# Kernel tuning notes

Hardware: AMD Instinct MI355X
Metric: run time of the kernel (lower is better)

## Reference

```python
import jax, jax.numpy as jnp
import numpy as np

B, TQ, TK = 2, 2048, 2048
H, E, D = 16, 256, 4096       # num_heads, embed_dim, d_model
DH = D // H                   # head_dim == embed_dim (required by per-head RMSNorm(embed_dim))
LAMBDA_INIT = 0.8
LAYER_INDEX = 0
EPS = 1.1920929e-07           # torch RMSNorm default eps = finfo(float32).eps


def setup_inputs() -> dict:
    key = jax.random.key(0)
    ks = jax.random.split(key, 14)
    s = 0.02
    lam_init_val = LAMBDA_INIT - 0.6 * float(np.exp(-0.3 * LAYER_INDEX))
    return {
        "x": jax.random.normal(ks[0], (B, TQ, E), jnp.float32),
        "encoder_out": jax.random.normal(ks[1], (B, TK, E), jnp.float32),
        "Wq": jax.random.normal(ks[2], (H, E, DH), jnp.float32) * s,
        "bq": jnp.zeros((H, DH), jnp.float32),
        "Wk": jax.random.normal(ks[3], (H, E, DH), jnp.float32) * s,
        "bk": jnp.zeros((H, DH), jnp.float32),
        "Wv": jax.random.normal(ks[4], (H, E, DH), jnp.float32) * s,
        "bv": jnp.zeros((H, DH), jnp.float32),
        "lq1": jax.random.normal(ks[5], (H, DH), jnp.float32) * 0.1,
        "lk1": jax.random.normal(ks[6], (H, DH), jnp.float32) * 0.1,
        "lq2": jax.random.normal(ks[7], (H, DH), jnp.float32) * 0.1,
        "lk2": jax.random.normal(ks[8], (H, DH), jnp.float32) * 0.1,
        "lam_init": jnp.full((H,), lam_init_val, jnp.float32),
        "g": jnp.ones((H, DH), jnp.float32),     # per-head RMSNorm weight
        "Wo": jax.random.normal(ks[9], (D, E), jnp.float32) * s,
        "bo": jnp.zeros((E,), jnp.float32),
    }


def reference(x, encoder_out, Wq, bq, Wk, bk, Wv, bv,
              lq1, lk1, lq2, lk2, lam_init, g, Wo, bo):
    # per-head projections, vectorized over heads: [B,H,T,DH]
    q = jnp.einsum('bte,hed->bhtd', x, Wq) + bq[:, None, :]
    k = jnp.einsum('bse,hed->bhsd', encoder_out, Wk) + bk[:, None, :]
    v = jnp.einsum('bse,hed->bhsd', encoder_out, Wv) + bv[:, None, :]
    dh2 = DH // 2
    q1, q2 = q[..., :dh2], q[..., dh2:]
    k1, k2 = k[..., :dh2], k[..., dh2:]
    scale = 1.0 / jnp.sqrt(jnp.float32(dh2))
    s1 = jax.nn.softmax(jnp.einsum('bhtd,bhsd->bhts', q1, k1) * scale, axis=-1)
    s2 = jax.nn.softmax(jnp.einsum('bhtd,bhsd->bhts', q2, k2) * scale, axis=-1)
    # learned per-head lambda scalar
    lam = jnp.exp(jnp.sum(lq1 * lk1, axis=-1)) - jnp.exp(jnp.sum(lq2 * lk2, axis=-1)) + lam_init  # [H]
    w = s1 - lam[None, :, None, None] * s2
    o = jnp.einsum('bhts,bhsd->bhtd', w, v)
    # per-head RMSNorm + (1 - lambda_init) scaling
    rms = jnp.sqrt(jnp.mean(o * o, axis=-1, keepdims=True) + EPS)
    o = (1.0 - LAMBDA_INIT) * (o / rms) * g[None, :, None, :]
    # concat heads -> output projection
    o = o.transpose(0, 2, 1, 3).reshape(B, TQ, D)
    return o @ Wo + bo
```

## Files before the change

### kernel.cpp

```cpp
#include <hip/hip_runtime.h>
#include <hip/hip_bf16.h>
#include <stdint.h>
#include <math.h>

typedef __bf16 bf16;
typedef __bf16 bf16x8 __attribute__((ext_vector_type(8)));
typedef float f32x4 __attribute__((ext_vector_type(4)));
typedef float f32x16 __attribute__((ext_vector_type(16)));
typedef unsigned int u32;

#define MFMA16(a, b, c) __builtin_amdgcn_mfma_f32_16x16x32_bf16(a, b, c, 0, 0, 0)
#define MFMA32(a, b, c) __builtin_amdgcn_mfma_f32_32x32x16_bf16(a, b, c, 0, 0, 0)

typedef const u32 __attribute__((address_space(1)))* gptr1;
typedef u32 __attribute__((address_space(3)))* lptr3;

__device__ __forceinline__ void load_lds16(const void* g, void* l) {
    __builtin_amdgcn_global_load_lds((gptr1)g, (lptr3)l, 16, 0, 0);
}

__device__ __forceinline__ u32 pk2(float lo, float hi_) {
    union { bf16 h[2]; u32 u; } t;
    t.h[0] = (bf16)lo; t.h[1] = (bf16)hi_;
    return t.u;
}
__device__ __forceinline__ u32 xswap(u32 x) {
    return (u32)__shfl_xor((int)x, 32);
}

#define SCALE_QK 0.08838834764831845f
#define LOG2E 1.4426950408889634f
#define QK_PRESCALE (SCALE_QK * LOG2E)
#define RMS_EPS 1.1920929e-07f
#define OUT_SCALE 0.2f
#define M0_BIAS (-16.0f)

__global__ void cvt_act(const float* __restrict__ x, const float* __restrict__ enc,
                        bf16* __restrict__ xb, bf16* __restrict__ eb) {
    int gid = blockIdx.x * 256 + threadIdx.x;
    const float* src = (gid < 131072) ? x : enc;
    bf16* dst = (gid < 131072) ? xb : eb;
    int i = (gid & 131071) * 8;
    float4 v0 = *(const float4*)(src + i);
    float4 v1 = *(const float4*)(src + i + 4);
    union { bf16 h[8]; uint4 u; } p;
    p.h[0] = (bf16)v0.x; p.h[1] = (bf16)v0.y; p.h[2] = (bf16)v0.z; p.h[3] = (bf16)v0.w;
    p.h[4] = (bf16)v1.x; p.h[5] = (bf16)v1.y; p.h[6] = (bf16)v1.z; p.h[7] = (bf16)v1.w;
    *(uint4*)(dst + i) = p.u;
}

__global__ void txp_w(const float* __restrict__ Wq, const float* __restrict__ Wk,
                      const float* __restrict__ Wv,
                      bf16* __restrict__ WTq, bf16* __restrict__ WTk, bf16* __restrict__ WTv) {
    int z = blockIdx.z; int iw = z >> 4, hh = z & 15;
    const float* src = (iw == 0 ? Wq : iw == 1 ? Wk : Wv) + hh * 65536;
    bf16* dst = (iw == 0 ? WTq : iw == 1 ? WTk : WTv) + hh * 65536;
    __shared__ bf16 T[64][68];
    int r0 = blockIdx.y * 64, c0 = blockIdx.x * 64;
    int tid = threadIdx.x;
#pragma unroll
    for (int t = 0; t < 4; ++t) {
        int idx = tid + t * 256;
        int row = idx >> 4, c4 = (idx & 15) * 4;
        float4 v = *(const float4*)(src + (r0 + row) * 256 + c0 + c4);
        T[row][c4] = (bf16)v.x; T[row][c4 + 1] = (bf16)v.y;
        T[row][c4 + 2] = (bf16)v.z; T[row][c4 + 3] = (bf16)v.w;
    }
    __syncthreads();
#pragma unroll
    for (int t = 0; t < 2; ++t) {
        int idx = tid + t * 256;
        int crow = idx >> 3, r8 = (idx & 7) * 8;
        union { bf16 h[8]; uint4 u; } p;
#pragma unroll
        for (int j = 0; j < 8; ++j) p.h[j] = T[r8 + j][crow];
        *(uint4*)(dst + (c0 + crow) * 256 + r0 + r8) = p.u;
    }
}

__global__ void txp_wo(const float* __restrict__ Wo, bf16* __restrict__ WoT) {
    __shared__ bf16 T[64][68];
    int r0 = blockIdx.y * 64, c0 = blockIdx.x * 64;
    int tid = threadIdx.x;
#pragma unroll
    for (int t = 0; t < 4; ++t) {
        int idx = tid + t * 256;
        int row = idx >> 4, c4 = (idx & 15) * 4;
        float4 v = *(const float4*)(Wo + (size_t)(r0 + row) * 256 + c0 + c4);
        T[row][c4] = (bf16)v.x; T[row][c4 + 1] = (bf16)v.y;
        T[row][c4 + 2] = (bf16)v.z; T[row][c4 + 3] = (bf16)v.w;
    }
    __syncthreads();
#pragma unroll
    for (int t = 0; t < 2; ++t) {
        int idx = tid + t * 256;
        int crow = idx >> 3, r8 = (idx & 7) * 8;
        union { bf16 h[8]; uint4 u; } p;
#pragma unroll
        for (int j = 0; j < 8; ++j) p.h[j] = T[r8 + j][crow];
        *(uint4*)(WoT + (size_t)(c0 + crow) * 4096 + r0 + r8) = p.u;
    }
}

__global__ void txp_v(const bf16* __restrict__ V, bf16* __restrict__ VT) {
    int bh = blockIdx.z;
    const bf16* src = V + (size_t)bh * 2048 * 256;
    bf16* dst = VT + (size_t)bh * 256 * 2048;
    __shared__ bf16 T[64][68];
    int s0 = blockIdx.x * 64, d0 = blockIdx.y * 64;
    int tid = threadIdx.x;
#pragma unroll
    for (int t = 0; t < 2; ++t) {
        int idx = tid + t * 256;
        int row = idx >> 3, c8 = (idx & 7) * 8;
        uint4 v = *(const uint4*)(src + (s0 + row) * 256 + d0 + c8);
        *(uint2*)&T[row][c8] = make_uint2(v.x, v.y);
        *(uint2*)&T[row][c8 + 4] = make_uint2(v.z, v.w);
    }
    __syncthreads();
#pragma unroll
    for (int t = 0; t < 2; ++t) {
        int idx = tid + t * 256;
        int crow = idx >> 3, r8 = (idx & 7) * 8;
        union { bf16 h[8]; uint4 u; } p;
#pragma unroll
        for (int j = 0; j < 8; ++j) p.h[j] = T[r8 + j][crow];
        *(uint4*)(dst + (d0 + crow) * 2048 + s0 + r8) = p.u;
    }
}

__global__ void lam_kernel(const float* __restrict__ lq1, const float* __restrict__ lk1,
                           const float* __restrict__ lq2, const float* __restrict__ lk2,
                           const float* __restrict__ lam_init, float* __restrict__ lam_out) {
    int tid = threadIdx.x; int hh = tid >> 4, i = tid & 15;
    float s1 = 0.f, s2 = 0.f;
#pragma unroll
    for (int j = 0; j < 16; ++j) {
        int d = i + j * 16;
        s1 += lq1[hh * 256 + d] * lk1[hh * 256 + d];
        s2 += lq2[hh * 256 + d] * lk2[hh * 256 + d];
    }
#pragma unroll
    for (int msk = 1; msk < 16; msk <<= 1) { s1 += __shfl_xor(s1, msk); s2 += __shfl_xor(s2, msk); }
    if (i == 0) lam_out[hh] = __expf(s1) - __expf(s2) + lam_init[hh];
}

__global__ __launch_bounds__(256) void proj_gemm(
    const bf16* __restrict__ xb, const bf16* __restrict__ eb,
    const bf16* __restrict__ WTq, const bf16* __restrict__ WTk, const bf16* __restrict__ WTv,
    const float* __restrict__ bq, const float* __restrict__ bk, const float* __restrict__ bv,
    bf16* __restrict__ Qb, bf16* __restrict__ Kb, bf16* __restrict__ Vb) {
    int z = blockIdx.z;
    const bf16* A = (z == 0) ? xb : eb;
    const bf16* BT = (z == 0) ? WTq : (z == 1) ? WTk : WTv;
    const float* bias = (z == 0) ? bq : (z == 1) ? bk : bv;
    bf16* out = (z == 0) ? Qb : (z == 1) ? Kb : Vb;
    float qs = (z == 0) ? QK_PRESCALE : 1.0f;

    __shared__ alignas(16) bf16 As[128 * 32];
    __shared__ alignas(16) bf16 Bs[128 * 32];
    int m0 = blockIdx.x * 128, n0 = blockIdx.y * 128;
    int tid = threadIdx.x, w = tid >> 6, lane = tid & 63;
    int lrow = lane & 15, lgrp = lane >> 4, lk8 = lgrp * 8;
    int wr = (w >> 1) * 64, wc = (w & 1) * 64;

    f32x4 acc[4][4];
#pragma unroll
    for (int i = 0; i < 4; ++i)
#pragma unroll
        for (int j = 0; j < 4; ++j) acc[i][j] = (f32x4){0.f, 0.f, 0.f, 0.f};

    for (int k0 = 0; k0 < 256; k0 += 32) {
        __syncthreads();
#pragma unroll
        for (int t = 0; t < 2; ++t) {
            int c = tid + t * 256;
            int row = c >> 2, k8 = (c & 3) * 8;
            load_lds16(A + (m0 + row) * 256 + k0 + k8, &As[c * 8]);
            load_lds16(BT + (n0 + row) * 256 + k0 + k8, &Bs[c * 8]);
        }
        __syncthreads();
        bf16x8 af[4], bfr[4];
#pragma unroll
        for (int f = 0; f < 4; ++f) af[f] = *(const bf16x8*)&As[(wr + f * 16 + lrow) * 32 + lk8];
#pragma unroll
        for (int f = 0; f < 4; ++f) bfr[f] = *(const bf16x8*)&Bs[(wc + f * 16 + lrow) * 32 + lk8];
#pragma unroll
        for (int i = 0; i < 4; ++i)
#pragma unroll
            for (int j = 0; j < 4; ++j) acc[i][j] = MFMA16(af[i], bfr[j], acc[i][j]);
    }
#pragma unroll
    for (int i = 0; i < 4; ++i) {
#pragma unroll
        for (int j = 0; j < 4; ++j) {
            int n = n0 + wc + j * 16 + lrow;
            float bvv = bias[n];
            int hh = n >> 8, d = n & 255;
#pragma unroll
            for (int r = 0; r < 4; ++r) {
                int m = m0 + wr + i * 16 + lgrp * 4 + r;
                int bb = m >> 11, tt = m & 2047;
                out[(((size_t)bb * 16 + hh) * 2048 + tt) * 256 + d] = (bf16)((acc[i][j][r] + bvv) * qs);
            }
        }
    }
}

__global__ __launch_bounds__(256, 2) void attn_kernel(
    const bf16* __restrict__ Qb, const bf16* __restrict__ Kb, const bf16* __restrict__ VTb,
    const float* __restrict__ lam_ws, const float* __restrict__ g, bf16* __restrict__ On) {
    __shared__ alignas(16) char SMEM[75264];
    bf16* KsB = (bf16*)SMEM;
    bf16* VsB = (bf16*)(SMEM + 32768);
    float* o2buf  = (float*)SMEM;
    float* smem_i = (float*)(SMEM + 65536);
    float* smem_r = (float*)(SMEM + 66048);
    float* psum   = (float*)(SMEM + 66560);

    int orig = blockIdx.x;
    int xcd = orig & 7, idx = orig >> 3;
    int bh = xcd * 4 + (idx >> 5);
    int qb = idx & 31;
    int b = bh >> 4, h = bh & 15;
    int q0 = qb * 64;

    int tid = threadIdx.x, w = tid >> 6, lane = tid & 63;
    int lq = lane & 31, hi = lane >> 5;
    int br = w >> 1, qw = (w & 1) * 32;
    int ksw = lq & 7;
    int vsw = (lq >> 1) & 3;
    bool hib = (hi != 0);

    const bf16* Qg = Qb + ((size_t)bh * 2048 + q0 + qw + lq) * 256 + br * 128;
    bf16x8 qf[8];
#pragma unroll
    for (int dk = 0; dk < 8; ++dk)
        qf[dk] = *(const bf16x8*)(Qg + dk * 16 + hi * 8);

    f32x16 o[8];
#pragma unroll
    for (int dt = 0; dt < 8; ++dt)
#pragma unroll
        for (int i = 0; i < 16; ++i) o[dt][i] = 0.f;
    float lsum = 0.f;

    const bf16* Kg = Kb + (size_t)bh * 2048 * 256;
    const bf16* VTg = VTb + (size_t)bh * 256 * 2048;

    auto STAGE = [&](int buf, int kt) {
        int s0 = kt * 32;
#pragma unroll
        for (int i = 0; i < 4; ++i) {
            int s = i * 256 + tid;
            int row = s >> 5;
            int cg = (s & 31) ^ (row & 7);
            load_lds16(Kg + (size_t)(s0 + row) * 256 + cg * 8, KsB + buf * 8192 + s * 8);
        }
#pragma unroll
        for (int i = 0; i < 4; ++i) {
            int s = i * 256 + tid;
            int row = s >> 2;
            int cg = (s & 3) ^ ((row >> 1) & 3);
            load_lds16(VTg + (size_t)row * 2048 + s0 + cg * 8, VsB + buf * 8192 + s * 8);
        }
    };

    STAGE(0, 0);
    __syncthreads();

    int cur = 0;
    for (int kt = 0; kt < 64; ++kt) {
        if (kt + 1 < 64) STAGE(cur ^ 1, kt + 1);
        const bf16* Kbuf = KsB + cur * 8192;
        const bf16* Vbuf = VsB + cur * 8192;

        f32x16 sa, sb;
#pragma unroll
        for (int i = 0; i < 16; ++i) { sa[i] = M0_BIAS; sb[i] = 0.f; }
        __builtin_amdgcn_s_setprio(1);
#pragma unroll
        for (int dk = 0; dk < 4; ++dk) {
            bf16x8 k0 = *(const bf16x8*)&Kbuf[lq * 256 + (((br * 16 + 4 * dk + hi) ^ ksw) << 3)];
            bf16x8 k1 = *(const bf16x8*)&Kbuf[lq * 256 + (((br * 16 + 4 * dk + 2 + hi) ^ ksw) << 3)];
            sa = MFMA32(k0, qf[2 * dk], sa);
            sb = MFMA32(k1, qf[2 * dk + 1], sb);
        }
        __builtin_amdgcn_s_setprio(0);

        float p[16];
        float ls0 = 0.f, ls1 = 0.f;
#pragma unroll
        for (int i = 0; i < 8; ++i) { p[i] = exp2f(sa[i] + sb[i]); ls0 += p[i]; }
#pragma unroll
        for (int i = 8; i < 16; ++i) { p[i] = exp2f(sa[i] + sb[i]); ls1 += p[i]; }
        lsum += ls0 + ls1;

        u32 X0 = pk2(p[0], p[1]),   X1 = pk2(p[2], p[3]);
        u32 Y0 = pk2(p[4], p[5]),   Y1 = pk2(p[6], p[7]);
        u32 Z0 = pk2(p[8], p[9]),   Z1 = pk2(p[10], p[11]);
        u32 W0 = pk2(p[12], p[13]), W1 = pk2(p[14], p[15]);
        u32 pX0 = xswap(X0), pX1 = xswap(X1);
        u32 pY0 = xswap(Y0), pY1 = xswap(Y1);
        u32 pZ0 = xswap(Z0), pZ1 = xswap(Z1);
        u32 pW0 = xswap(W0), pW1 = xswap(W1);
        union { u32 u[4]; bf16x8 v; } PA0, PA1;
        PA0.u[0] = hib ? pY0 : X0;  PA0.u[1] = hib ? pY1 : X1;
        PA0.u[2] = hib ? Y0 : pX0;  PA0.u[3] = hib ? Y1 : pX1;
        PA1.u[0] = hib ? pW0 : Z0;  PA1.u[1] = hib ? pW1 : Z1;
        PA1.u[2] = hib ? W0 : pZ0;  PA1.u[3] = hib ? W1 : pZ1;

        __builtin_amdgcn_s_setprio(1);
#pragma unroll
        for (int dt = 0; dt < 8; ++dt) {
            const bf16* vrow = &Vbuf[(dt * 32 + lq) * 32];
            bf16x8 v0 = *(const bf16x8*)&vrow[(hi ^ vsw) << 3];
            o[dt] = MFMA32(PA0.v, v0, o[dt]);
            bf16x8 v1 = *(const bf16x8*)&vrow[((2 + hi) ^ vsw) << 3];
            o[dt] = MFMA32(PA1.v, v1, o[dt]);
        }
        __builtin_amdgcn_s_setprio(0);

        __syncthreads();
        cur ^= 1;
    }

    lsum += __shfl_xor(lsum, 32);
    float lam = lam_ws[h];
    float inv = (br == 0) ? 1.f / lsum : lam / lsum;
    smem_i[br * 64 + qw + lq] = inv;
    __syncthreads();

    if (br == 1) {
#pragma unroll
        for (int r = 0; r < 16; ++r) {
            int qp = (r & 3) + 8 * (r >> 2) + 4 * hi + qw;
            float i2 = smem_i[64 + qp];
#pragma unroll
            for (int dt = 0; dt < 8; ++dt)
                o2buf[qp * 256 + dt * 32 + lq] = o[dt][r] * i2;
        }
    }
    __syncthreads();

    if (br == 0) {
#pragma unroll
        for (int r = 0; r < 16; ++r) {
            int qp = (r & 3) + 8 * (r >> 2) + 4 * hi + qw;
            float i1 = smem_i[qp];
            float ss = 0.f;
#pragma unroll
            for (int dt = 0; dt < 8; ++dt) {
                float v = o[dt][r] * i1 - o2buf[qp * 256 + dt * 32 + lq];
                o[dt][r] = v;
                ss += v * v;
            }
            psum[qp * 33 + lq] = ss;
        }
    }
    __syncthreads();

    if (tid < 64) {
        float s = 0.f;
#pragma unroll
        for (int i = 0; i < 32; ++i) s += psum[tid * 33 + i];
        smem_r[tid] = 1.f / sqrtf(s * (1.f / 256.f) + RMS_EPS);
    }
    __syncthreads();

    if (br == 0) {
        float gv[8];
#pragma unroll
        for (int dt = 0; dt < 8; ++dt) gv[dt] = g[h * 256 + dt * 32 + lq] * OUT_SCALE;
#pragma unroll
        for (int r = 0; r < 16; ++r) {
            int qp = (r & 3) + 8 * (r >> 2) + 4 * hi + qw;
            float rv = smem_r[qp];
            size_t base = ((size_t)b * 2048 + q0 + qp) * 4096 + h * 256;
#pragma unroll
            for (int dt = 0; dt < 8; ++dt)
                On[base + dt * 32 + lq] = (bf16)(o[dt][r] * rv * gv[dt]);
        }
    }
}

__global__ __launch_bounds__(256) void out_gemm(const bf16* __restrict__ A, const bf16* __restrict__ BT,
                                                const float* __restrict__ bo, float* __restrict__ out) {
    __shared__ alignas(16) bf16 As[64 * 32];
    __shared__ alignas(16) bf16 Bs[64 * 32];
    int m0 = blockIdx.x * 64, n0 = blockIdx.y * 64;
    int tid = threadIdx.x, w = tid >> 6, lane = tid & 63;
    int lrow = lane & 15, lgrp = lane >> 4, lk8 = lgrp * 8;
    int wr = (w >> 1) * 32, wc = (w & 1) * 32;
    f32x4 acc[2][2];
#pragma unroll
    for (int i = 0; i < 2; ++i)
#pragma unroll
        for (int j = 0; j < 2; ++j) acc[i][j] = (f32x4){0.f, 0.f, 0.f, 0.f};
    for (int k0 = 0; k0 < 4096; k0 += 32) {
        __syncthreads();
        int row = tid >> 2, k8 = (tid & 3) * 8;
        load_lds16(A + (size_t)(m0 + row) * 4096 + k0 + k8, &As[tid * 8]);
        load_lds16(BT + (size_t)(n0 + row) * 4096 + k0 + k8, &Bs[tid * 8]);
        __syncthreads();
        bf16x8 af[2], bfr[2];
#pragma unroll
        for (int f = 0; f < 2; ++f) {
            af[f] = *(const bf16x8*)&As[(wr + f * 16 + lrow) * 32 + lk8];
            bfr[f] = *(const bf16x8*)&Bs[(wc + f * 16 + lrow) * 32 + lk8];
        }
#pragma unroll
        for (int i = 0; i < 2; ++i)
#pragma unroll
            for (int j = 0; j < 2; ++j) acc[i][j] = MFMA16(af[i], bfr[j], acc[i][j]);
    }
#pragma unroll
    for (int i = 0; i < 2; ++i)
#pragma unroll
        for (int j = 0; j < 2; ++j) {
            int n = n0 + wc + j * 16 + lrow;
            float bv = bo[n];
#pragma unroll
            for (int r = 0; r < 4; ++r) {
                int m = m0 + wr + i * 16 + lgrp * 4 + r;
                out[(size_t)m * 256 + n] = acc[i][j][r] + bv;
            }
        }
}

extern "C" void kernel_launch(void* const* d_in, const int* in_sizes, int n_in,
                              void* d_out, int out_size, void* d_ws, size_t ws_size,
                              hipStream_t stream) {
    const float* x = (const float*)d_in[0];
    const float* enc = (const float*)d_in[1];
    const float* Wq = (const float*)d_in[2];
    const float* bq = (const float*)d_in[3];
    const float* Wk = (const float*)d_in[4];
    const float* bk = (const float*)d_in[5];
    const float* Wv = (const float*)d_in[6];
    const float* bv = (const float*)d_in[7];
    const float* lq1 = (const float*)d_in[8];
    const float* lk1 = (const float*)d_in[9];
    const float* lq2 = (const float*)d_in[10];
    const float* lk2 = (const float*)d_in[11];
    const float* lam_init = (const float*)d_in[12];
    const float* g = (const float*)d_in[13];
    const float* Wo = (const float*)d_in[14];
    const float* bo = (const float*)d_in[15];
    float* out = (float*)d_out;

    char* ws = (char*)d_ws;
    const size_t MB = 1024 * 1024;
    bf16* xb  = (bf16*)(ws + 0 * MB);
    bf16* eb  = (bf16*)(ws + 2 * MB);
    bf16* WTq = (bf16*)(ws + 4 * MB);
    bf16* WTk = (bf16*)(ws + 6 * MB);
    bf16* WTv = (bf16*)(ws + 8 * MB);
    bf16* WoT = (bf16*)(ws + 10 * MB);
    float* lam = (float*)(ws + 12 * MB);
    bf16* Qb  = (bf16*)(ws + 13 * MB);
    bf16* Kb  = (bf16*)(ws + 45 * MB);
    bf16* Vb  = (bf16*)(ws + 77 * MB);
    bf16* VTb = (bf16*)(ws + 109 * MB);
    bf16* On  = Vb;

    hipLaunchKernelGGL(cvt_act, dim3(1024), dim3(256), 0, stream, x, enc, xb, eb);
    hipLaunchKernelGGL(txp_w, dim3(4, 4, 48), dim3(256), 0, stream, Wq, Wk, Wv, WTq, WTk, WTv);
    hipLaunchKernelGGL(txp_wo, dim3(4, 64, 1), dim3(256), 0, stream, Wo, WoT);
    hipLaunchKernelGGL(lam_kernel, dim3(1), dim3(256), 0, stream, lq1, lk1, lq2, lk2, lam_init, lam);
    hipLaunchKernelGGL(proj_gemm, dim3(32, 32, 3), dim3(256), 0, stream,
                       xb, eb, WTq, WTk, WTv, bq, bk, bv, Qb, Kb, Vb);
    hipLaunchKernelGGL(txp_v, dim3(32, 4, 32), dim3(256), 0, stream, Vb, VTb);
    hipLaunchKernelGGL(attn_kernel, dim3(1024), dim3(256), 0, stream, Qb, Kb, VTb, lam, g, On);
    hipLaunchKernelGGL(out_gemm, dim3(64, 4), dim3(256), 0, stream, On, WoT, bo, out);
}
```

Before: 362.0 us.

## Write V transposed from projection GEMM with permuted key order, drop txp_v and shuffles

The projection GEMM epilogue for V now writes directly into the transposed VT layout, with a lane-group permutation on the key index so each MFMA lane's P values already line up with the matching V columns. This removes the separate txp_v kernel launch and its full read and write of V. It also removes the cross-half lane shuffles and selects used to rearrange P before the PV MFMA. The cost is narrower 8-byte strided stores in the GEMM epilogue, and correctness depends on the key permutation matching the attention kernel's MFMA fragment layout.

```diff
diff --git a/kernel.cpp b/kernel.cpp
--- a/kernel.cpp
+++ b/kernel.cpp
@@ -23,9 +23,6 @@
     union { bf16 h[2]; u32 u; } t;
     t.h[0] = (bf16)lo; t.h[1] = (bf16)hi_;
     return t.u;
-}
-__device__ __forceinline__ u32 xswap(u32 x) {
-    return (u32)__shfl_xor((int)x, 32);
 }
 
 #define SCALE_QK 0.08838834764831845f
@@ -102,33 +99,6 @@
     }
 }
 
-__global__ void txp_v(const bf16* __restrict__ V, bf16* __restrict__ VT) {
-    int bh = blockIdx.z;
-    const bf16* src = V + (size_t)bh * 2048 * 256;
-    bf16* dst = VT + (size_t)bh * 256 * 2048;
-    __shared__ bf16 T[64][68];
-    int s0 = blockIdx.x * 64, d0 = blockIdx.y * 64;
-    int tid = threadIdx.x;
-#pragma unroll
-    for (int t = 0; t < 2; ++t) {
-        int idx = tid + t * 256;
-        int row = idx >> 3, c8 = (idx & 7) * 8;
-        uint4 v = *(const uint4*)(src + (s0 + row) * 256 + d0 + c8);
-        *(uint2*)&T[row][c8] = make_uint2(v.x, v.y);
-        *(uint2*)&T[row][c8 + 4] = make_uint2(v.z, v.w);
-    }
-    __syncthreads();
-#pragma unroll
-    for (int t = 0; t < 2; ++t) {
-        int idx = tid + t * 256;
-        int crow = idx >> 3, r8 = (idx & 7) * 8;
-        union { bf16 h[8]; uint4 u; } p;
-#pragma unroll
-        for (int j = 0; j < 8; ++j) p.h[j] = T[r8 + j][crow];
-        *(uint4*)(dst + (d0 + crow) * 2048 + s0 + r8) = p.u;
-    }
-}
-
 __global__ void lam_kernel(const float* __restrict__ lq1, const float* __restrict__ lk1,
                            const float* __restrict__ lq2, const float* __restrict__ lk2,
                            const float* __restrict__ lam_init, float* __restrict__ lam_out) {
@@ -149,12 +119,12 @@
     const bf16* __restrict__ xb, const bf16* __restrict__ eb,
     const bf16* __restrict__ WTq, const bf16* __restrict__ WTk, const bf16* __restrict__ WTv,
     const float* __restrict__ bq, const float* __restrict__ bk, const float* __restrict__ bv,
-    bf16* __restrict__ Qb, bf16* __restrict__ Kb, bf16* __restrict__ Vb) {
+    bf16* __restrict__ Qb, bf16* __restrict__ Kb, bf16* __restrict__ VTb) {
     int z = blockIdx.z;
     const bf16* A = (z == 0) ? xb : eb;
     const bf16* BT = (z == 0) ? WTq : (z == 1) ? WTk : WTv;
     const float* bias = (z == 0) ? bq : (z == 1) ? bk : bv;
-    bf16* out = (z == 0) ? Qb : (z == 1) ? Kb : Vb;
+    bf16* out = (z == 0) ? Qb : Kb;
     float qs = (z == 0) ? QK_PRESCALE : 1.0f;
 
     __shared__ alignas(16) bf16 As[128 * 32];
@@ -190,18 +160,38 @@
 #pragma unroll
             for (int j = 0; j < 4; ++j) acc[i][j] = MFMA16(af[i], bfr[j], acc[i][j]);
     }
-#pragma unroll
-    for (int i = 0; i < 4; ++i) {
-#pragma unroll
-        for (int j = 0; j < 4; ++j) {
-            int n = n0 + wc + j * 16 + lrow;
-            float bvv = bias[n];
-            int hh = n >> 8, d = n & 255;
-#pragma unroll
-            for (int r = 0; r < 4; ++r) {
-                int m = m0 + wr + i * 16 + lgrp * 4 + r;
-                int bb = m >> 11, tt = m & 2047;
-                out[(((size_t)bb * 16 + hh) * 2048 + tt) * 256 + d] = (bf16)((acc[i][j][r] + bvv) * qs);
+
+    if (z == 2) {
+        int lg2 = ((lgrp & 1) << 1) | (lgrp >> 1);
+#pragma unroll
+        for (int i = 0; i < 4; ++i) {
+            int m_ = m0 + wr + i * 16;
+            int bb = m_ >> 11, tb = m_ & 2047;
+#pragma unroll
+            for (int j = 0; j < 4; ++j) {
+                int n = n0 + wc + j * 16 + lrow;
+                float bvv = bias[n];
+                int hh = n >> 8, d = n & 255;
+                union { bf16 h[4]; uint2 u2; } pk;
+#pragma unroll
+                for (int r = 0; r < 4; ++r) pk.h[r] = (bf16)(acc[i][j][r] + bvv);
+                *(uint2*)(VTb + (((size_t)bb * 16 + hh) * 256 + d) * 2048 + tb + lg2 * 4) = pk.u2;
+            }
+        }
+    } else {
+#pragma unroll
+        for (int i = 0; i < 4; ++i) {
+#pragma unroll
+            for (int j = 0; j < 4; ++j) {
+                int n = n0 + wc + j * 16 + lrow;
+                float bvv = bias[n];
+                int hh = n >> 8, d = n & 255;
+#pragma unroll
+                for (int r = 0; r < 4; ++r) {
+                    int m = m0 + wr + i * 16 + lgrp * 4 + r;
+                    int bb = m >> 11, tt = m & 2047;
+                    out[(((size_t)bb * 16 + hh) * 2048 + tt) * 256 + d] = (bf16)((acc[i][j][r] + bvv) * qs);
+                }
             }
         }
     }
@@ -230,7 +220,6 @@
     int br = w >> 1, qw = (w & 1) * 32;
     int ksw = lq & 7;
     int vsw = (lq >> 1) & 3;
-    bool hib = (hi != 0);
 
     const bf16* Qg = Qb + ((size_t)bh * 2048 + q0 + qw + lq) * 256 + br * 128;
     bf16x8 qf[8];
@@ -296,19 +285,11 @@
         for (int i = 8; i < 16; ++i) { p[i] = exp2f(sa[i] + sb[i]); ls1 += p[i]; }
         lsum += ls0 + ls1;
 
-        u32 X0 = pk2(p[0], p[1]),   X1 = pk2(p[2], p[3]);
-        u32 Y0 = pk2(p[4], p[5]),   Y1 = pk2(p[6], p[7]);
-        u32 Z0 = pk2(p[8], p[9]),   Z1 = pk2(p[10], p[11]);
-        u32 W0 = pk2(p[12], p[13]), W1 = pk2(p[14], p[15]);
-        u32 pX0 = xswap(X0), pX1 = xswap(X1);
-        u32 pY0 = xswap(Y0), pY1 = xswap(Y1);
-        u32 pZ0 = xswap(Z0), pZ1 = xswap(Z1);
-        u32 pW0 = xswap(W0), pW1 = xswap(W1);
         union { u32 u[4]; bf16x8 v; } PA0, PA1;
-        PA0.u[0] = hib ? pY0 : X0;  PA0.u[1] = hib ? pY1 : X1;
-        PA0.u[2] = hib ? Y0 : pX0;  PA0.u[3] = hib ? Y1 : pX1;
-        PA1.u[0] = hib ? pW0 : Z0;  PA1.u[1] = hib ? pW1 : Z1;
-        PA1.u[2] = hib ? W0 : pZ0;  PA1.u[3] = hib ? W1 : pZ1;
+        PA0.u[0] = pk2(p[0], p[1]);   PA0.u[1] = pk2(p[2], p[3]);
+        PA0.u[2] = pk2(p[4], p[5]);   PA0.u[3] = pk2(p[6], p[7]);
+        PA1.u[0] = pk2(p[8], p[9]);   PA1.u[1] = pk2(p[10], p[11]);
+        PA1.u[2] = pk2(p[12], p[13]); PA1.u[3] = pk2(p[14], p[15]);
 
         __builtin_amdgcn_s_setprio(1);
 #pragma unroll
@@ -460,17 +441,15 @@
     float* lam = (float*)(ws + 12 * MB);
     bf16* Qb  = (bf16*)(ws + 13 * MB);
     bf16* Kb  = (bf16*)(ws + 45 * MB);
-    bf16* Vb  = (bf16*)(ws + 77 * MB);
+    bf16* On  = (bf16*)(ws + 77 * MB);
     bf16* VTb = (bf16*)(ws + 109 * MB);
-    bf16* On  = Vb;
 
     hipLaunchKernelGGL(cvt_act, dim3(1024), dim3(256), 0, stream, x, enc, xb, eb);
     hipLaunchKernelGGL(txp_w, dim3(4, 4, 48), dim3(256), 0, stream, Wq, Wk, Wv, WTq, WTk, WTv);
     hipLaunchKernelGGL(txp_wo, dim3(4, 64, 1), dim3(256), 0, stream, Wo, WoT);
     hipLaunchKernelGGL(lam_kernel, dim3(1), dim3(256), 0, stream, lq1, lk1, lq2, lk2, lam_init, lam);
     hipLaunchKernelGGL(proj_gemm, dim3(32, 32, 3), dim3(256), 0, stream,
-                       xb, eb, WTq, WTk, WTv, bq, bk, bv, Qb, Kb, Vb);
-    hipLaunchKernelGGL(txp_v, dim3(32, 4, 32), dim3(256), 0, stream, Vb, VTb);
+                       xb, eb, WTq, WTk, WTv, bq, bk, bv, Qb, Kb, VTb);
     hipLaunchKernelGGL(attn_kernel, dim3(1024), dim3(256), 0, stream, Qb, Kb, VTb, lam, g, On);
     hipLaunchKernelGGL(out_gemm, dim3(64, 4), dim3(256), 0, stream, On, WoT, bo, out);
 }
```

After: 349.2 us. -3.5%, faster.
